# Kernel optimization log

Measured on AMD Instinct MI355X. Metric: run time of the kernel, lower is better.

## Reference

```python
import jax, jax.numpy as jnp
import numpy as np

B, H, S = 32, 128, 8192

def setup_inputs() -> dict:
    key = jax.random.key(0)
    k1, k2, k3, k4, k5 = jax.random.split(key, 5)
    return {
        "static_hidden": jax.random.normal(k1, (B, H, S), dtype=jnp.float32),
        "dynamic_hidden": jax.random.normal(k2, (B, H, S), dtype=jnp.float32),
        "decoder_hidden": jax.random.normal(k3, (B, H), dtype=jnp.float32),
        "v": jax.random.normal(k4, (1, 1, H), dtype=jnp.float32) * 0.01,
        "W": jax.random.normal(k5, (1, H, 3 * H), dtype=jnp.float32) * 0.01,
    }

def reference(static_hidden, dynamic_hidden, decoder_hidden, v, W):
    b, h, s = static_hidden.shape
    # concat (static, dynamic, expanded decoder) along feature dim -> [b, 3h, s]
    hidden = jnp.concatenate(
        [static_hidden, dynamic_hidden,
         jnp.broadcast_to(decoder_hidden[:, :, None], (b, h, s))], axis=1)
    # W[0]: [h, 3h]; tanh(W @ hidden) -> [b, h, s]
    e = jnp.tanh(jnp.einsum('hk,bks->bhs', W[0], hidden))
    # v[0,0]: [h]; scores -> [b, 1, s]
    scores = jnp.einsum('h,bhs->bs', v[0, 0], e)[:, None, :]
    return jax.nn.softmax(scores, axis=2)
```

## Files before the change

kernel.cpp:

```cpp
#include <hip/hip_runtime.h>
#include <math.h>

#define BB 32
#define HH 128
#define SS 8192

typedef __attribute__((ext_vector_type(8))) short bf8;
typedef __attribute__((ext_vector_type(4))) float f4;

static __device__ __forceinline__ unsigned short f2bf(float x) {
  union { float f; unsigned int u; } c; c.f = x;
  unsigned int r = c.u + 0x7FFFu + ((c.u >> 16) & 1u);
  return (unsigned short)(r >> 16);
}

#define XSWZ(r) ((((r) >> 2) ^ (r)) & 7)

__global__ __launch_bounds__(256) void prep_kernel(
    const float* __restrict__ W, const float* __restrict__ dec,
    unsigned short* __restrict__ Abf, float* __restrict__ bias) {
  const int b = blockIdx.x;
  const int tid = threadIdx.x;
  if (tid < HH) {
    const float* wr = W + (size_t)tid * 384 + 256;
    const float* db = dec + (size_t)b * HH;
    float acc = 0.f;
    #pragma unroll 8
    for (int j = 0; j < HH; ++j) acc += wr[j] * db[j];
    bias[b * HH + tid] = acc;
  }
  if (b == 0) {
    #pragma unroll 4
    for (int idx = tid; idx < HH * 256; idx += 256) {
      int h = idx >> 8, k = idx & 255;
      Abf[idx] = f2bf(W[h * 384 + k]);
    }
  }
}

__global__ __launch_bounds__(1024, 4) void attn_main(
    const float* __restrict__ sta, const float* __restrict__ dyn,
    const unsigned short* __restrict__ Abf, const float* __restrict__ bias,
    const float* __restrict__ v, float* __restrict__ scores) {
  extern __shared__ __align__(16) unsigned short smem[];
  unsigned short* LA = smem;
  unsigned short* LX = smem + 32768;

  const int tid  = threadIdx.x;
  const int l    = tid & 63;
  const int w    = tid >> 6;
  const int quad = l >> 4;
  const int n16  = l & 15;
  const int b       = blockIdx.x >> 3;
  const int sb_base = (blockIdx.x & 7) << 2;

  const int kq = ((w >> 2) << 4) + (quad << 2);
  const int sl = ((w & 3) << 6) + (n16 << 2);
  const size_t xoff_b = (size_t)b * HH * SS;

  f4 g[2][4];

  auto issueX = [&](int t, f4* gg) {
    const int c = t & 3;
    const float* base = (c < 2) ? sta : dyn;
    const float* p = base + xoff_b + (size_t)(((c & 1) << 6) + kq) * SS
                   + (((sb_base + (t >> 2)) << 8) + sl);
    #pragma unroll
    for (int j = 0; j < 4; ++j) gg[j] = *(const f4*)(p + (size_t)j * SS);
  };
  auto convWrite = [&](const f4* gg, int buf) {
    unsigned short* X = LX + (buf << 14);
    #pragma unroll
    for (int i = 0; i < 4; ++i) {
      const int srow = sl + i;
      ushort4 o;
      o.x = f2bf(gg[0][i]); o.y = f2bf(gg[1][i]);
      o.z = f2bf(gg[2][i]); o.w = f2bf(gg[3][i]);
      *(ushort4*)&X[(srow << 6) + ((((kq >> 3) ^ XSWZ(srow)) << 3) | (kq & 7))] = o;
    }
  };

  issueX(0, g[0]);
  #pragma unroll
  for (int j = 0; j < 4; ++j) {
    int gc = (j << 10) + tid;
    int m = gc >> 5, ck = gc & 31;
    bf8 val = *(const bf8*)(Abf + ((size_t)gc << 3));
    *(bf8*)&LA[(m << 8) + ((ck ^ (m & 7)) << 3)] = val;
  }
  issueX(1, g[1]);
  convWrite(g[0], 0);
  __syncthreads();

  f4 acc[8];
  #pragma unroll
  for (int mt = 0; mt < 8; ++mt) acc[mt] = (f4){0.f, 0.f, 0.f, 0.f};

  const int srow_f = (w << 4) + n16;
  const int xrow = srow_f << 6;
  const int sswz = XSWZ(srow_f);
  const int aswz = n16 & 7;

  for (int strip = 0; strip < 4; ++strip) {
    #pragma unroll
    for (int c = 0; c < 4; ++c) {
      const int t = (strip << 2) + c;
      if (t + 2 < 16) issueX(t + 2, g[c & 1]);
      const unsigned short* X = LX + ((c & 1) << 14);
      bf8 bf0 = *(const bf8*)&X[xrow + ((quad ^ sswz) << 3)];
      bf8 bf1 = *(const bf8*)&X[xrow + (((4 + quad) ^ sswz) << 3)];
      #pragma unroll
      for (int mt = 0; mt < 8; ++mt) {
        const int arow = (mt << 4) + n16;
        bf8 a0 = *(const bf8*)&LA[(arow << 8) + ((((c << 3) + quad) ^ aswz) << 3)];
        acc[mt] = __builtin_amdgcn_mfma_f32_16x16x32_bf16(a0, bf0, acc[mt], 0, 0, 0);
        bf8 a1 = *(const bf8*)&LA[(arow << 8) + ((((c << 3) + 4 + quad) ^ aswz) << 3)];
        acc[mt] = __builtin_amdgcn_mfma_f32_16x16x32_bf16(a1, bf1, acc[mt], 0, 0, 0);
      }
      if (t + 1 < 16) convWrite(g[(c + 1) & 1], (c + 1) & 1);
      if (c == 3) {
        float part = 0.f;
        #pragma unroll
        for (int mt = 0; mt < 8; ++mt) {
          #pragma unroll
          for (int r = 0; r < 4; ++r) {
            const int h = (mt << 4) + (quad << 2) + r;
            part += v[h] * tanhf(acc[mt][r] + bias[(b << 7) + h]);
            acc[mt][r] = 0.f;
          }
        }
        part += __shfl_xor(part, 16, 64);
        part += __shfl_xor(part, 32, 64);
        if (quad == 0)
          scores[((size_t)b << 13) + (((sb_base + strip) << 8) + srow_f)] = part;
      }
      __syncthreads();
    }
  }
}

__global__ __launch_bounds__(1024) void softmax_kernel(float* __restrict__ out) {
  const int b = blockIdx.x;
  const int tid = threadIdx.x;
  float* row = out + ((size_t)b << 13);
  float4 x0 = ((const float4*)row)[tid];
  float4 x1 = ((const float4*)row)[tid + 1024];
  float lmax = fmaxf(fmaxf(fmaxf(x0.x, x0.y), fmaxf(x0.z, x0.w)),
                     fmaxf(fmaxf(x1.x, x1.y), fmaxf(x1.z, x1.w)));
  __shared__ float red[17];
  #pragma unroll
  for (int o = 32; o >= 1; o >>= 1) lmax = fmaxf(lmax, __shfl_xor(lmax, o, 64));
  if ((tid & 63) == 0) red[tid >> 6] = lmax;
  __syncthreads();
  if (tid < 64) {
    float m = (tid < 16) ? red[tid] : -3.0e38f;
    #pragma unroll
    for (int o = 8; o >= 1; o >>= 1) m = fmaxf(m, __shfl_xor(m, o, 64));
    if (tid == 0) red[16] = m;
  }
  __syncthreads();
  const float gmax = red[16];
  float e[8];
  e[0] = expf(x0.x - gmax); e[1] = expf(x0.y - gmax);
  e[2] = expf(x0.z - gmax); e[3] = expf(x0.w - gmax);
  e[4] = expf(x1.x - gmax); e[5] = expf(x1.y - gmax);
  e[6] = expf(x1.z - gmax); e[7] = expf(x1.w - gmax);
  float ls = e[0] + e[1] + e[2] + e[3] + e[4] + e[5] + e[6] + e[7];
  #pragma unroll
  for (int o = 32; o >= 1; o >>= 1) ls += __shfl_xor(ls, o, 64);
  __syncthreads();
  if ((tid & 63) == 0) red[tid >> 6] = ls;
  __syncthreads();
  if (tid < 64) {
    float m = (tid < 16) ? red[tid] : 0.f;
    #pragma unroll
    for (int o = 8; o >= 1; o >>= 1) m += __shfl_xor(m, o, 64);
    if (tid == 0) red[16] = m;
  }
  __syncthreads();
  const float inv = 1.0f / red[16];
  float4 o0 = make_float4(e[0] * inv, e[1] * inv, e[2] * inv, e[3] * inv);
  float4 o1 = make_float4(e[4] * inv, e[5] * inv, e[6] * inv, e[7] * inv);
  ((float4*)row)[tid] = o0;
  ((float4*)row)[tid + 1024] = o1;
}

extern "C" void kernel_launch(void* const* d_in, const int* in_sizes, int n_in,
                              void* d_out, int out_size, void* d_ws, size_t ws_size,
                              hipStream_t stream) {
  const float* sta = (const float*)d_in[0];
  const float* dyn = (const float*)d_in[1];
  const float* dec = (const float*)d_in[2];
  const float* v   = (const float*)d_in[3];
  const float* W   = (const float*)d_in[4];

  unsigned short* Abf = (unsigned short*)d_ws;
  float* bias = (float*)((char*)d_ws + 128 * 256 * 2);
  float* scores = (float*)d_out;

  static bool attr_done = false;
  if (!attr_done) {
    (void)hipFuncSetAttribute((const void*)attn_main,
                              hipFuncAttributeMaxDynamicSharedMemorySize, 131072);
    attr_done = true;
  }

  prep_kernel<<<BB, 256, 0, stream>>>(W, dec, Abf, bias);
  attn_main<<<BB * 8, 1024, 131072, stream>>>(sta, dyn, Abf, bias, v, scores);
  softmax_kernel<<<BB, 1024, 0, stream>>>(scores);
}
```

Before: 385.5 us.

## Stream X tiles directly to LDS via global_load_lds, convert to bf16 at read

Replaces the register-staged global loads with bf16 conversion and swizzled LDS writes by direct global-to-LDS DMA (global_load_lds, 16 bytes per lane) of fp32 tiles. Conversion to bf16 now happens when each wave reads its B operand from LDS, using eight strided scalar reads per MFMA step. The K loop is restructured into 8 chunks of 32 with one MFMA per tile per chunk, and v and bias are cached in LDS. The aim is to free VGPRs and cut the load/convert/write overhead, at the cost of a barrier per chunk (twice as many syncs), unswizzled strided LDS reads that may bank-conflict, and slightly more LDS.

```diff
diff --git a/kernel.cpp b/kernel.cpp
--- a/kernel.cpp
+++ b/kernel.cpp
@@ -14,7 +14,11 @@
   return (unsigned short)(r >> 16);
 }
 
-#define XSWZ(r) ((((r) >> 2) ^ (r)) & 7)
+typedef const __attribute__((address_space(1))) void gv_t;
+typedef __attribute__((address_space(3))) void lv_t;
+static __device__ __forceinline__ void gll16(const float* g, float* l) {
+  __builtin_amdgcn_global_load_lds((gv_t*)g, (lv_t*)l, 16, 0, 0);
+}
 
 __global__ __launch_bounds__(256) void prep_kernel(
     const float* __restrict__ W, const float* __restrict__ dec,
@@ -38,13 +42,15 @@
   }
 }
 
-__global__ __launch_bounds__(1024, 4) void attn_main(
+__global__ __launch_bounds__(1024) void attn_main(
     const float* __restrict__ sta, const float* __restrict__ dyn,
     const unsigned short* __restrict__ Abf, const float* __restrict__ bias,
     const float* __restrict__ v, float* __restrict__ scores) {
-  extern __shared__ __align__(16) unsigned short smem[];
-  unsigned short* LA = smem;
-  unsigned short* LX = smem + 32768;
+  extern __shared__ __align__(16) unsigned char smem[];
+  unsigned short* LA = (unsigned short*)smem;
+  float* LX = (float*)(smem + 65536);
+  float* vL = (float*)(smem + 131072);
+  float* biasL = vL + HH;
 
   const int tid  = threadIdx.x;
   const int l    = tid & 63;
@@ -54,33 +60,21 @@
   const int b       = blockIdx.x >> 3;
   const int sb_base = (blockIdx.x & 7) << 2;
 
-  const int kq = ((w >> 2) << 4) + (quad << 2);
-  const int sl = ((w & 3) << 6) + (n16 << 2);
   const size_t xoff_b = (size_t)b * HH * SS;
 
-  f4 g[2][4];
-
-  auto issueX = [&](int t, f4* gg) {
-    const int c = t & 3;
-    const float* base = (c < 2) ? sta : dyn;
-    const float* p = base + xoff_b + (size_t)(((c & 1) << 6) + kq) * SS
-                   + (((sb_base + (t >> 2)) << 8) + sl);
-    #pragma unroll
-    for (int j = 0; j < 4; ++j) gg[j] = *(const f4*)(p + (size_t)j * SS);
+  auto issue = [&](int t) {
+    const int strip = sb_base + (t >> 3);
+    const int kc = t & 7;
+    const float* mat = (kc < 4) ? sta : dyn;
+    const int rr = w << 1;
+    const float* g = mat + xoff_b + (size_t)(((kc & 3) << 5) + rr) * SS
+                   + (strip << 8) + (l << 2);
+    float* lp = LX + ((t & 1) << 13) + (rr << 8);
+    gll16(g, lp);
+    gll16(g + SS, lp + 256);
   };
-  auto convWrite = [&](const f4* gg, int buf) {
-    unsigned short* X = LX + (buf << 14);
-    #pragma unroll
-    for (int i = 0; i < 4; ++i) {
-      const int srow = sl + i;
-      ushort4 o;
-      o.x = f2bf(gg[0][i]); o.y = f2bf(gg[1][i]);
-      o.z = f2bf(gg[2][i]); o.w = f2bf(gg[3][i]);
-      *(ushort4*)&X[(srow << 6) + ((((kq >> 3) ^ XSWZ(srow)) << 3) | (kq & 7))] = o;
-    }
-  };
-
-  issueX(0, g[0]);
+
+  issue(0);
   #pragma unroll
   for (int j = 0; j < 4; ++j) {
     int gc = (j << 10) + tid;
@@ -88,51 +82,56 @@
     bf8 val = *(const bf8*)(Abf + ((size_t)gc << 3));
     *(bf8*)&LA[(m << 8) + ((ck ^ (m & 7)) << 3)] = val;
   }
-  issueX(1, g[1]);
-  convWrite(g[0], 0);
+  if (tid < HH) {
+    vL[tid] = v[tid];
+    biasL[tid] = bias[(b << 7) + tid];
+  }
   __syncthreads();
 
   f4 acc[8];
   #pragma unroll
   for (int mt = 0; mt < 8; ++mt) acc[mt] = (f4){0.f, 0.f, 0.f, 0.f};
 
-  const int srow_f = (w << 4) + n16;
-  const int xrow = srow_f << 6;
-  const int sswz = XSWZ(srow_f);
+  const int srow = (w << 4) + n16;
   const int aswz = n16 & 7;
 
-  for (int strip = 0; strip < 4; ++strip) {
+  #pragma unroll
+  for (int strip4 = 0; strip4 < 4; ++strip4) {
     #pragma unroll
-    for (int c = 0; c < 4; ++c) {
-      const int t = (strip << 2) + c;
-      if (t + 2 < 16) issueX(t + 2, g[c & 1]);
-      const unsigned short* X = LX + ((c & 1) << 14);
-      bf8 bf0 = *(const bf8*)&X[xrow + ((quad ^ sswz) << 3)];
-      bf8 bf1 = *(const bf8*)&X[xrow + (((4 + quad) ^ sswz) << 3)];
+    for (int kc = 0; kc < 8; ++kc) {
+      const int t = (strip4 << 3) + kc;
+      if (t < 31) issue(t + 1);
+
+      const float* X = LX + ((t & 1) << 13);
+      float xf[8];
+      #pragma unroll
+      for (int j = 0; j < 8; ++j) xf[j] = X[(((quad << 3) + j) << 8) + srow];
+      bf8 xb;
+      #pragma unroll
+      for (int j = 0; j < 8; ++j) xb[j] = (short)f2bf(xf[j]);
+
       #pragma unroll
       for (int mt = 0; mt < 8; ++mt) {
         const int arow = (mt << 4) + n16;
-        bf8 a0 = *(const bf8*)&LA[(arow << 8) + ((((c << 3) + quad) ^ aswz) << 3)];
-        acc[mt] = __builtin_amdgcn_mfma_f32_16x16x32_bf16(a0, bf0, acc[mt], 0, 0, 0);
-        bf8 a1 = *(const bf8*)&LA[(arow << 8) + ((((c << 3) + 4 + quad) ^ aswz) << 3)];
-        acc[mt] = __builtin_amdgcn_mfma_f32_16x16x32_bf16(a1, bf1, acc[mt], 0, 0, 0);
+        bf8 af = *(const bf8*)&LA[(arow << 8) + ((((kc << 2) + quad) ^ aswz) << 3)];
+        acc[mt] = __builtin_amdgcn_mfma_f32_16x16x32_bf16(af, xb, acc[mt], 0, 0, 0);
       }
-      if (t + 1 < 16) convWrite(g[(c + 1) & 1], (c + 1) & 1);
-      if (c == 3) {
+
+      if (kc == 7) {
         float part = 0.f;
         #pragma unroll
         for (int mt = 0; mt < 8; ++mt) {
           #pragma unroll
           for (int r = 0; r < 4; ++r) {
             const int h = (mt << 4) + (quad << 2) + r;
-            part += v[h] * tanhf(acc[mt][r] + bias[(b << 7) + h]);
+            part += vL[h] * tanhf(acc[mt][r] + biasL[h]);
             acc[mt][r] = 0.f;
           }
         }
         part += __shfl_xor(part, 16, 64);
         part += __shfl_xor(part, 32, 64);
         if (quad == 0)
-          scores[((size_t)b << 13) + (((sb_base + strip) << 8) + srow_f)] = part;
+          scores[((size_t)b << 13) + (((sb_base + strip4) << 8) + srow)] = part;
       }
       __syncthreads();
     }
@@ -201,11 +200,11 @@
   static bool attr_done = false;
   if (!attr_done) {
     (void)hipFuncSetAttribute((const void*)attn_main,
-                              hipFuncAttributeMaxDynamicSharedMemorySize, 131072);
+                              hipFuncAttributeMaxDynamicSharedMemorySize, 132096);
     attr_done = true;
   }
 
   prep_kernel<<<BB, 256, 0, stream>>>(W, dec, Abf, bias);
-  attn_main<<<BB * 8, 1024, 131072, stream>>>(sta, dyn, Abf, bias, v, scores);
+  attn_main<<<BB * 8, 1024, 132096, stream>>>(sta, dyn, Abf, bias, v, scores);
   softmax_kernel<<<BB, 1024, 0, stream>>>(scores);
 }
```

Result: faster. 367.7 us (-4.6%).
